# Kernel optimization log

Hardware: AMD Instinct MI355X
Metric: run time of the kernel (lower is better)

## Reference

```python
import jax, jax.numpy as jnp
import numpy as np

EMBED_DIM = 1024
NUM_HEADS = 16
HEAD_DIM = EMBED_DIM // NUM_HEADS


def setup_inputs() -> dict:
    key = jax.random.key(0)
    ks = jax.random.split(key, 5)
    B, N, E = 2, 2048, EMBED_DIM
    scale = E ** -0.5
    return {
        "x": jax.random.normal(ks[0], (B, N, E), dtype=jnp.float32),
        "w_qkv": jax.random.normal(ks[1], (E, 3 * E), dtype=jnp.float32) * scale,
        "b_qkv": jnp.zeros((3 * E,), dtype=jnp.float32),
        "w_proj": jax.random.normal(ks[2], (E, E), dtype=jnp.float32) * scale,
        "b_proj": jnp.zeros((E,), dtype=jnp.float32),
    }


def reference(x, w_qkv, b_qkv, w_proj, b_proj):
    B, N, E = x.shape
    H, D = NUM_HEADS, HEAD_DIM
    qkv = x @ w_qkv + b_qkv                      # [B,N,3E]
    qkv = qkv.reshape(B, N, 3, H, D)
    q = qkv[:, :, 0].transpose(0, 2, 1, 3)        # [B,H,N,D]
    k = qkv[:, :, 1].transpose(0, 2, 1, 3)
    v = qkv[:, :, 2].transpose(0, 2, 1, 3)
    attn = jnp.einsum('bhnd,bhmd->bhnm', q, k) * (D ** -0.5)
    attn = jax.nn.softmax(attn, axis=-1)          # dropout is identity in eval mode
    out = jnp.einsum('bhnm,bhmd->bhnd', attn, v)  # [B,H,N,D]
    out = out.transpose(0, 2, 1, 3).reshape(B, N, E)
    return out @ w_proj + b_proj
```

## Files before the change

### kernel.cpp

```cpp
#include <hip/hip_runtime.h>
#include <hip/hip_bf16.h>
#include <cstdint>
#include <cstddef>


typedef __attribute__((ext_vector_type(8))) short short8;
typedef __attribute__((ext_vector_type(4))) short short4v;
typedef __attribute__((ext_vector_type(4))) float f32x4;

#define MFMA16(a, b, c) __builtin_amdgcn_mfma_f32_16x16x32_bf16((a), (b), (c), 0, 0, 0)
#define EXP2F(x) __builtin_amdgcn_exp2f(x)

__device__ __forceinline__ float b2f(short s) {
  union { unsigned u; float f; } x; x.u = ((unsigned)(unsigned short)s) << 16; return x.f;
}
__device__ __forceinline__ short f2b(float f) {
  union { __hip_bfloat16 h; short s; } u; u.h = __float2bfloat16(f); return u.s;
}
__device__ __forceinline__ void async_lds16(const void* g, void* l) {
  __builtin_amdgcn_global_load_lds(
      (const __attribute__((address_space(1))) void*)g,
      (__attribute__((address_space(3))) void*)l, 16, 0, 0);
}

__global__ __launch_bounds__(256) void cast_f32_bf16(const float* __restrict__ in,
                                                     short* __restrict__ out, int n4) {
  int idx = blockIdx.x * 256 + threadIdx.x;
  if (idx < n4) {
    f32x4 v = ((const f32x4*)in)[idx];
    short4v o;
    #pragma unroll
    for (int e = 0; e < 4; ++e) o[e] = f2b(v[e]);
    ((short4v*)out)[idx] = o;
  }
}

__global__ __launch_bounds__(256) void transpose_cast(const float* __restrict__ in,
                                                      short* __restrict__ out,
                                                      int R, int C) {
  __shared__ float tile[32][33];
  int c0 = blockIdx.x * 32, r0 = blockIdx.y * 32;
  int tx = threadIdx.x, ty = threadIdx.y;
  #pragma unroll
  for (int i = ty; i < 32; i += 8)
    tile[i][tx] = in[(size_t)(r0 + i) * C + c0 + tx];
  __syncthreads();
  #pragma unroll
  for (int i = ty; i < 32; i += 8)
    out[(size_t)(c0 + i) * R + r0 + tx] = f2b(tile[tx][i]);
}

__global__ __launch_bounds__(256, 3) void gemm_qkv(const short* __restrict__ xb,
                                                   const short* __restrict__ wT,
                                                   const float* __restrict__ bias,
                                                   short* __restrict__ Qb,
                                                   short* __restrict__ Kb,
                                                   short* __restrict__ Vt) {
  __shared__ short lds_a[128 * 64];
  __shared__ short lds_b[128 * 64];
  const int tid = threadIdx.x, wid = tid >> 6, lane = tid & 63;
  const int lg = lane >> 4, lr = lane & 15;
  const int lin = blockIdx.x;
  const int swz = (lin & 7) * 96 + (lin >> 3);
  const int m0 = (swz & 31) * 128, n0 = (swz >> 5) * 128;
  const int wr = wid >> 1, wc = wid & 1;
  const int K = 1024;
  const int sm = lr & 7;

  f32x4 acc[4][4];
  #pragma unroll
  for (int i = 0; i < 4; ++i)
    #pragma unroll
    for (int j = 0; j < 4; ++j) acc[i][j] = (f32x4)0.0f;

  for (int k0 = 0; k0 < K; k0 += 64) {
    #pragma unroll
    for (int it = 0; it < 4; ++it) {
      int chunk = it * 256 + tid;
      int row = chunk >> 3, kc = ((chunk & 7) ^ (row & 7)) * 8;
      async_lds16(xb + (size_t)(m0 + row) * K + k0 + kc, lds_a + chunk * 8);
      async_lds16(wT + (size_t)(n0 + row) * K + k0 + kc, lds_b + chunk * 8);
    }
    __syncthreads();
    #pragma unroll
    for (int kk = 0; kk < 2; ++kk) {
      short8 af[4], bfr[4];
      #pragma unroll
      for (int i = 0; i < 4; ++i)
        af[i] = *(const short8*)&lds_a[(wr * 64 + i * 16 + lr) * 64 +
                                       (((kk * 4 + lg) ^ sm) * 8)];
      #pragma unroll
      for (int j = 0; j < 4; ++j)
        bfr[j] = *(const short8*)&lds_b[(wc * 64 + j * 16 + lr) * 64 +
                                        (((kk * 4 + lg) ^ sm) * 8)];
      #pragma unroll
      for (int i = 0; i < 4; ++i)
        #pragma unroll
        for (int j = 0; j < 4; ++j) acc[i][j] = MFMA16(af[i], bfr[j], acc[i][j]);
    }
    __syncthreads();
  }

  #pragma unroll
  for (int i = 0; i < 4; ++i) {
    int gm = m0 + wr * 64 + i * 16 + lg * 4;
    int bb = gm >> 11, n = gm & 2047;
    #pragma unroll
    for (int j = 0; j < 4; ++j) {
      int gc = n0 + wc * 64 + j * 16 + lr;
      float bv = bias[gc];
      int which = gc >> 10;
      int h = (gc >> 6) & 15;
      int dd = gc & 63;
      size_t qkbase = ((size_t)((bb * 16 + h) * 2048 + n)) * 64 + dd;
      if (which == 2) {
        size_t vtbase = ((size_t)((bb * 16 + h) * 64 + dd)) * 2048 + n;
        short4v pv;
        #pragma unroll
        for (int r = 0; r < 4; ++r) pv[r] = f2b(acc[i][j][r] + bv);
        *(short4v*)&Vt[vtbase] = pv;
      } else {
        short* dst = (which == 0) ? Qb : Kb;
        #pragma unroll
        for (int r = 0; r < 4; ++r)
          dst[qkbase + (size_t)r * 64] = f2b(acc[i][j][r] + bv);
      }
    }
  }
}

__global__ __launch_bounds__(512) void attn_fwd(const short* __restrict__ Qb,
                                                const short* __restrict__ Kb,
                                                const short* __restrict__ Vt,
                                                short* __restrict__ aob) {
  __shared__ short k_lds[2][64 * 64];
  __shared__ short v_lds[2][64 * 64];
  __shared__ short p_lds[8 * 16 * 64];
  const int tid = threadIdx.x, wid = tid >> 6, lane = tid & 63;
  const int lg = lane >> 4, lr = lane & 15;
  const int lin = blockIdx.x;
  const int swz = (lin & 7) * 64 + (lin >> 3);
  const int qt = swz & 15, bh = swz >> 4;
  const int q0 = qt * 128 + wid * 16;
  const short* Qbh = Qb + (size_t)bh * 2048 * 64;
  const short* Kbh = Kb + (size_t)bh * 2048 * 64;
  const short* Vbh = Vt + (size_t)bh * 64 * 2048;
  const int rm = (lr >> 1) & 7;

  const int srow = tid >> 3;
  const int ssrc = ((tid & 7) ^ ((srow >> 1) & 7)) * 8;

  int pw[4], pr[2];
  #pragma unroll
  for (int jt = 0; jt < 4; ++jt)
    pw[jt] = wid * 1024 + lr * 64 + (((jt * 2 + (lg >> 1)) ^ rm) * 8) + (lg & 1) * 4;
  #pragma unroll
  for (int kk = 0; kk < 2; ++kk)
    pr[kk] = wid * 1024 + lr * 64 + (((kk * 4 + lg) ^ rm) * 8);

  short8 qf[2];
  #pragma unroll
  for (int kk = 0; kk < 2; ++kk) {
    qf[kk] = *(const short8*)(Qbh + (size_t)(q0 + lr) * 64 + kk * 32 + lg * 8);
    #pragma unroll
    for (int e = 0; e < 8; ++e) qf[kk][e] = f2b(b2f(qf[kk][e]) * 0.1803368801f);
  }

  f32x4 o[4];
  #pragma unroll
  for (int dt = 0; dt < 4; ++dt) o[dt] = (f32x4)0.0f;
  float m_ = -__builtin_inff(), l_ = 0.0f;

  async_lds16(Kbh + (size_t)srow * 64 + ssrc, &k_lds[0][tid * 8]);
  async_lds16(Vbh + (size_t)srow * 2048 + 0 + ssrc, &v_lds[0][tid * 8]);
  asm volatile("s_waitcnt vmcnt(0)" ::: "memory");
  __syncthreads();

  for (int t = 0; t < 32; ++t) {
    const int cur = t & 1;
    if (t + 1 < 32) {
      int kvn = (t + 1) * 64;
      async_lds16(Kbh + (size_t)(kvn + srow) * 64 + ssrc, &k_lds[cur ^ 1][tid * 8]);
      async_lds16(Vbh + (size_t)srow * 2048 + kvn + ssrc, &v_lds[cur ^ 1][tid * 8]);
    }

    f32x4 s[4];
    #pragma unroll
    for (int jt = 0; jt < 4; ++jt) s[jt] = (f32x4)0.0f;
    #pragma unroll
    for (int jt = 0; jt < 4; ++jt)
      #pragma unroll
      for (int kk = 0; kk < 2; ++kk) {
        short8 kf = *(const short8*)&k_lds[cur][(jt * 16 + lr) * 64 +
                                               (((kk * 4 + lg) ^ rm) * 8)];
        s[jt] = MFMA16(kf, qf[kk], s[jt]);
      }

    float mj[4];
    #pragma unroll
    for (int jt = 0; jt < 4; ++jt)
      mj[jt] = fmaxf(fmaxf(s[jt][0], s[jt][1]), fmaxf(s[jt][2], s[jt][3]));
    float pmax = fmaxf(fmaxf(mj[0], mj[1]), fmaxf(mj[2], mj[3]));
    pmax = fmaxf(pmax, __shfl_xor(pmax, 16));
    pmax = fmaxf(pmax, __shfl_xor(pmax, 32));
    if (!__all(pmax - m_ <= 8.0f)) {
      float mn = fmaxf(m_, pmax);
      float corr = EXP2F(m_ - mn);
      m_ = mn;
      l_ *= corr;
      #pragma unroll
      for (int dt = 0; dt < 4; ++dt)
        #pragma unroll
        for (int r = 0; r < 4; ++r) o[dt][r] *= corr;
    }

    float psj[4];
    #pragma unroll
    for (int jt = 0; jt < 4; ++jt) {
      float p0 = EXP2F(s[jt][0] - m_), p1 = EXP2F(s[jt][1] - m_);
      float p2 = EXP2F(s[jt][2] - m_), p3 = EXP2F(s[jt][3] - m_);
      short4v pv;
      pv[0] = f2b(p0); pv[1] = f2b(p1); pv[2] = f2b(p2); pv[3] = f2b(p3);
      *(short4v*)&p_lds[pw[jt]] = pv;
      psj[jt] = (p0 + p1) + (p2 + p3);
    }
    float ps = (psj[0] + psj[1]) + (psj[2] + psj[3]);
    ps += __shfl_xor(ps, 16);
    ps += __shfl_xor(ps, 32);
    l_ += ps;

    asm volatile("s_waitcnt lgkmcnt(0)" ::: "memory");
    __builtin_amdgcn_sched_barrier(0);

    #pragma unroll
    for (int kk = 0; kk < 2; ++kk) {
      short8 pa = *(const short8*)&p_lds[pr[kk]];
      #pragma unroll
      for (int dt = 0; dt < 4; ++dt) {
        short8 vb = *(const short8*)&v_lds[cur][(dt * 16 + lr) * 64 +
                                               (((kk * 4 + lg) ^ rm) * 8)];
        o[dt] = MFMA16(vb, pa, o[dt]);
      }
    }
    asm volatile("s_waitcnt vmcnt(0)" ::: "memory");
    __syncthreads();
  }

  const int bb = bh >> 4, h = bh & 15;
  const float inv_l = __frcp_rn(l_);
  #pragma unroll
  for (int dt = 0; dt < 4; ++dt) {
    short4v ov;
    #pragma unroll
    for (int r = 0; r < 4; ++r) ov[r] = f2b(o[dt][r] * inv_l);
    *(short4v*)&aob[(size_t)(bb * 2048 + q0 + lr) * 1024 + h * 64 + dt * 16 + lg * 4] = ov;
  }
}

__global__ __launch_bounds__(256, 2) void gemm_proj(const short* __restrict__ aob,
                                                    const short* __restrict__ wT,
                                                    const float* __restrict__ bias,
                                                    float* __restrict__ out) {
  __shared__ short lds_a[64 * 64];
  __shared__ short lds_b[128 * 64];
  const int tid = threadIdx.x, wid = tid >> 6, lane = tid & 63;
  const int lg = lane >> 4, lr = lane & 15;
  const int lin = blockIdx.x;
  const int swz = (lin & 7) * 64 + (lin >> 3);
  const int m0 = (swz & 63) * 64, n0 = (swz >> 6) * 128;
  const int mw = wid >> 1, nw = wid & 1;
  const int K = 1024;
  const int sm = lr & 7;

  f32x4 acc[2][4];
  #pragma unroll
  for (int i = 0; i < 2; ++i)
    #pragma unroll
    for (int j = 0; j < 4; ++j) acc[i][j] = (f32x4)0.0f;

  for (int k0 = 0; k0 < K; k0 += 64) {
    #pragma unroll
    for (int it = 0; it < 2; ++it) {
      int chunk = it * 256 + tid;
      int row = chunk >> 3, kc = ((chunk & 7) ^ (row & 7)) * 8;
      async_lds16(aob + (size_t)(m0 + row) * K + k0 + kc, lds_a + chunk * 8);
    }
    #pragma unroll
    for (int it = 0; it < 4; ++it) {
      int chunk = it * 256 + tid;
      int row = chunk >> 3, kc = ((chunk & 7) ^ (row & 7)) * 8;
      async_lds16(wT + (size_t)(n0 + row) * K + k0 + kc, lds_b + chunk * 8);
    }
    __syncthreads();
    #pragma unroll
    for (int kk = 0; kk < 2; ++kk) {
      short8 af[2], bfr[4];
      #pragma unroll
      for (int i = 0; i < 2; ++i)
        af[i] = *(const short8*)&lds_a[(mw * 32 + i * 16 + lr) * 64 +
                                       (((kk * 4 + lg) ^ sm) * 8)];
      #pragma unroll
      for (int j = 0; j < 4; ++j)
        bfr[j] = *(const short8*)&lds_b[(nw * 64 + j * 16 + lr) * 64 +
                                        (((kk * 4 + lg) ^ sm) * 8)];
      #pragma unroll
      for (int i = 0; i < 2; ++i)
        #pragma unroll
        for (int j = 0; j < 4; ++j) acc[i][j] = MFMA16(af[i], bfr[j], acc[i][j]);
    }
    __syncthreads();
  }

  #pragma unroll
  for (int i = 0; i < 2; ++i) {
    int gm = m0 + mw * 32 + i * 16 + lg * 4;
    #pragma unroll
    for (int j = 0; j < 4; ++j) {
      int gc = n0 + nw * 64 + j * 16 + lr;
      float bv = bias[gc];
      #pragma unroll
      for (int r = 0; r < 4; ++r)
        out[(size_t)(gm + r) * 1024 + gc] = acc[i][j][r] + bv;
    }
  }
}

extern "C" void kernel_launch(void* const* d_in, const int* in_sizes, int n_in,
                              void* d_out, int out_size, void* d_ws, size_t ws_size,
                              hipStream_t stream) {
  const float* x     = (const float*)d_in[0];
  const float* wqkv  = (const float*)d_in[1];
  const float* bqkv  = (const float*)d_in[2];
  const float* wproj = (const float*)d_in[3];
  const float* bproj = (const float*)d_in[4];
  float* out = (float*)d_out;

  char* ws = (char*)d_ws;
  short* xb     = (short*)ws; ws += (size_t)4096 * 1024 * 2;
  short* wqkvT  = (short*)ws; ws += (size_t)3072 * 1024 * 2;
  short* wprojT = (short*)ws; ws += (size_t)1024 * 1024 * 2;
  short* Qb     = (short*)ws; ws += (size_t)32 * 2048 * 64 * 2;
  short* Kb     = (short*)ws; ws += (size_t)32 * 2048 * 64 * 2;
  short* Vt     = (short*)ws; ws += (size_t)32 * 64 * 2048 * 2;
  short* aob    = (short*)ws; ws += (size_t)4096 * 1024 * 2;

  cast_f32_bf16<<<4096, 256, 0, stream>>>(x, xb, 4096 * 1024 / 4);
  transpose_cast<<<dim3(96, 32), dim3(32, 8), 0, stream>>>(wqkv, wqkvT, 1024, 3072);
  transpose_cast<<<dim3(32, 32), dim3(32, 8), 0, stream>>>(wproj, wprojT, 1024, 1024);
  gemm_qkv<<<768, 256, 0, stream>>>(xb, wqkvT, bqkv, Qb, Kb, Vt);
  attn_fwd<<<512, 512, 0, stream>>>(Qb, Kb, Vt, aob);
  gemm_proj<<<512, 256, 0, stream>>>(aob, wprojT, bproj, out);
}
```

Measured before the change: 193.9 us.

## Compute softmax row sum via MFMA with ones; enlarge transpose tiles; grid-stride cast

The attention kernel now accumulates the softmax denominator by running an extra MFMA of a bf16 ones vector against the P tile. This replaces the per-tile float sums, cross-lane shuffles and the lgkmcnt wait plus sched barrier. The denominator is then summed from the same bf16-rounded probabilities used for P·V. Separately, the weight transpose-cast uses 64x64 tiles with 256 flat threads, and the input cast becomes a grid-stride loop over 1024 blocks, both to cut launch and block overhead in the preprocessing kernels.

```diff
diff --git a/kernel.cpp b/kernel.cpp
--- a/kernel.cpp
+++ b/kernel.cpp
@@ -25,8 +25,7 @@
 
 __global__ __launch_bounds__(256) void cast_f32_bf16(const float* __restrict__ in,
                                                      short* __restrict__ out, int n4) {
-  int idx = blockIdx.x * 256 + threadIdx.x;
-  if (idx < n4) {
+  for (int idx = blockIdx.x * 256 + threadIdx.x; idx < n4; idx += 1024 * 256) {
     f32x4 v = ((const f32x4*)in)[idx];
     short4v o;
     #pragma unroll
@@ -38,15 +37,15 @@
 __global__ __launch_bounds__(256) void transpose_cast(const float* __restrict__ in,
                                                       short* __restrict__ out,
                                                       int R, int C) {
-  __shared__ float tile[32][33];
-  int c0 = blockIdx.x * 32, r0 = blockIdx.y * 32;
-  int tx = threadIdx.x, ty = threadIdx.y;
-  #pragma unroll
-  for (int i = ty; i < 32; i += 8)
+  __shared__ float tile[64][65];
+  int c0 = blockIdx.x * 64, r0 = blockIdx.y * 64;
+  int tx = threadIdx.x & 63, ty = threadIdx.x >> 6;
+  #pragma unroll
+  for (int i = ty; i < 64; i += 4)
     tile[i][tx] = in[(size_t)(r0 + i) * C + c0 + tx];
   __syncthreads();
   #pragma unroll
-  for (int i = ty; i < 32; i += 8)
+  for (int i = ty; i < 64; i += 4)
     out[(size_t)(c0 + i) * R + r0 + tx] = f2b(tile[tx][i]);
 }
 
@@ -158,6 +157,10 @@
   for (int kk = 0; kk < 2; ++kk)
     pr[kk] = wid * 1024 + lr * 64 + (((kk * 4 + lg) ^ rm) * 8);
 
+  short8 ones;
+  #pragma unroll
+  for (int e = 0; e < 8; ++e) ones[e] = (short)0x3F80;
+
   short8 qf[2];
   #pragma unroll
   for (int kk = 0; kk < 2; ++kk) {
@@ -166,10 +169,11 @@
     for (int e = 0; e < 8; ++e) qf[kk][e] = f2b(b2f(qf[kk][e]) * 0.1803368801f);
   }
 
-  f32x4 o[4];
+  f32x4 o[4], o_l;
   #pragma unroll
   for (int dt = 0; dt < 4; ++dt) o[dt] = (f32x4)0.0f;
-  float m_ = -__builtin_inff(), l_ = 0.0f;
+  o_l = (f32x4)0.0f;
+  float m_ = -__builtin_inff();
 
   async_lds16(Kbh + (size_t)srow * 64 + ssrc, &k_lds[0][tid * 8]);
   async_lds16(Vbh + (size_t)srow * 2048 + 0 + ssrc, &v_lds[0][tid * 8]);
@@ -207,34 +211,28 @@
       float mn = fmaxf(m_, pmax);
       float corr = EXP2F(m_ - mn);
       m_ = mn;
-      l_ *= corr;
       #pragma unroll
       for (int dt = 0; dt < 4; ++dt)
         #pragma unroll
         for (int r = 0; r < 4; ++r) o[dt][r] *= corr;
-    }
-
-    float psj[4];
+      #pragma unroll
+      for (int r = 0; r < 4; ++r) o_l[r] *= corr;
+    }
+
     #pragma unroll
     for (int jt = 0; jt < 4; ++jt) {
-      float p0 = EXP2F(s[jt][0] - m_), p1 = EXP2F(s[jt][1] - m_);
-      float p2 = EXP2F(s[jt][2] - m_), p3 = EXP2F(s[jt][3] - m_);
       short4v pv;
-      pv[0] = f2b(p0); pv[1] = f2b(p1); pv[2] = f2b(p2); pv[3] = f2b(p3);
+      pv[0] = f2b(EXP2F(s[jt][0] - m_));
+      pv[1] = f2b(EXP2F(s[jt][1] - m_));
+      pv[2] = f2b(EXP2F(s[jt][2] - m_));
+      pv[3] = f2b(EXP2F(s[jt][3] - m_));
       *(short4v*)&p_lds[pw[jt]] = pv;
-      psj[jt] = (p0 + p1) + (p2 + p3);
-    }
-    float ps = (psj[0] + psj[1]) + (psj[2] + psj[3]);
-    ps += __shfl_xor(ps, 16);
-    ps += __shfl_xor(ps, 32);
-    l_ += ps;
-
-    asm volatile("s_waitcnt lgkmcnt(0)" ::: "memory");
-    __builtin_amdgcn_sched_barrier(0);
+    }
 
     #pragma unroll
     for (int kk = 0; kk < 2; ++kk) {
       short8 pa = *(const short8*)&p_lds[pr[kk]];
+      o_l = MFMA16(ones, pa, o_l);
       #pragma unroll
       for (int dt = 0; dt < 4; ++dt) {
         short8 vb = *(const short8*)&v_lds[cur][(dt * 16 + lr) * 64 +
@@ -247,7 +245,7 @@
   }
 
   const int bb = bh >> 4, h = bh & 15;
-  const float inv_l = __frcp_rn(l_);
+  const float inv_l = __frcp_rn(o_l[0]);
   #pragma unroll
   for (int dt = 0; dt < 4; ++dt) {
     short4v ov;
@@ -344,9 +342,9 @@
   short* Vt     = (short*)ws; ws += (size_t)32 * 64 * 2048 * 2;
   short* aob    = (short*)ws; ws += (size_t)4096 * 1024 * 2;
 
-  cast_f32_bf16<<<4096, 256, 0, stream>>>(x, xb, 4096 * 1024 / 4);
-  transpose_cast<<<dim3(96, 32), dim3(32, 8), 0, stream>>>(wqkv, wqkvT, 1024, 3072);
-  transpose_cast<<<dim3(32, 32), dim3(32, 8), 0, stream>>>(wproj, wprojT, 1024, 1024);
+  cast_f32_bf16<<<1024, 256, 0, stream>>>(x, xb, 4096 * 1024 / 4);
+  transpose_cast<<<dim3(48, 16), 256, 0, stream>>>(wqkv, wqkvT, 1024, 3072);
+  transpose_cast<<<dim3(16, 16), 256, 0, stream>>>(wproj, wprojT, 1024, 1024);
   gemm_qkv<<<768, 256, 0, stream>>>(xb, wqkvT, bqkv, Qb, Kb, Vt);
   attn_fwd<<<512, 512, 0, stream>>>(Qb, Kb, Vt, aob);
   gemm_proj<<<512, 256, 0, stream>>>(aob, wprojT, bproj, out);
```

After: 192.0 us. Within noise of the previous version (-1.0%).
